# Performance work log

Hardware: AMD Instinct MI355X
Metric: run time of the kernel (lower is better)

## Reference

```python
import jax, jax.numpy as jnp
import numpy as np

N_NODES = 100000
N_EDGES = 1600000
D_FEAT = 128
UNITS = 128


def setup_inputs() -> dict:
    key = jax.random.key(0)
    k = jax.random.split(key, 7)
    x = jax.random.normal(k[0], (N_NODES, D_FEAT), dtype=jnp.float32)
    edge_row = jax.random.randint(k[1], (N_EDGES,), 0, N_NODES, dtype=jnp.int32)
    edge_col = jax.random.randint(k[2], (N_EDGES,), 0, N_NODES, dtype=jnp.int32)
    edge_vals = jax.random.uniform(k[3], (N_EDGES,), dtype=jnp.float32)
    W = jax.random.normal(k[4], (D_FEAT, UNITS), dtype=jnp.float32) * 0.05
    W_gate = jax.random.normal(k[5], (D_FEAT, 1), dtype=jnp.float32) * 0.05
    b_gate = jax.random.normal(k[6], (1,), dtype=jnp.float32) * 0.05
    return {"x": x, "edge_row": edge_row, "edge_col": edge_col,
            "edge_vals": edge_vals, "W": W, "W_gate": W_gate, "b_gate": b_gate}


def reference(x, edge_row, edge_col, edge_vals, W, W_gate, b_gate):
    # pre_sup = X @ W  -> [N, units]
    pre_sup = x @ W
    # gate g = sigmoid(X @ W_gate + b_gate)  -> [N, 1]
    g = jax.nn.sigmoid(x @ W_gate + b_gate)
    h = g * pre_sup  # [N, units]
    # output = A @ h, A in COO form (row, col, vals):
    # out[r] = sum_e vals[e] * h[col[e]] for edges with row[e] == r
    msgs = edge_vals[:, None] * h[edge_col]  # [E, units]
    out = jax.ops.segment_sum(msgs, edge_row, num_segments=N_NODES)
    # activation is None (linear)
    return out
```

## Files before the change

kernel.cpp:

```cpp
#include <hip/hip_runtime.h>
#include <hip/hip_bf16.h>

constexpr int D        = 128;
constexpr int BM       = 64;
constexpr int CHUNK    = 4096;
constexpr int NBKT_PAD = 1024;
constexpr int BKT_CAP  = 3072;
constexpr int BKT_STRIDE = 4096;
constexpr int OVF_CAP  = 65536;
constexpr int EPT      = CHUNK / 256;

typedef __attribute__((ext_vector_type(8))) short bf16x8;
typedef __attribute__((ext_vector_type(4))) float f32x4;

__device__ __forceinline__ unsigned short rne_bf16(float f) {
    unsigned u = __float_as_uint(f);
    return (unsigned short)((u + 0x7FFF + ((u >> 16) & 1)) >> 16);
}

__global__ __launch_bounds__(256) void transpose_W(
    const float* __restrict__ W, unsigned short* __restrict__ wt_sw)
{
    int idx = blockIdx.x * 256 + threadIdx.x;
    int k = idx >> 7, f = idx & 127;
    wt_sw[f * 128 + (k ^ ((f & 7) << 3))] = rne_bf16(W[idx]);
}

__global__ __launch_bounds__(256) void gemm_bin(
    const float* __restrict__ x, const unsigned short* __restrict__ wt_sw,
    const float* __restrict__ Wg, const float* __restrict__ bg,
    __hip_bfloat16* __restrict__ h,
    const int* __restrict__ er, const int* __restrict__ ec,
    const float* __restrict__ ev, int* __restrict__ gcursor,
    uint2* __restrict__ bucketArr, int* __restrict__ ovfCur,
    uint4* __restrict__ ovfArr,
    int n_nodes, int n_edges, int gemm_blocks)
{
    __shared__ __align__(16) char smem[53264];

    const int t    = threadIdx.x;
    const int lane = t & 63;
    const int w    = t >> 6;

    if ((int)blockIdx.x < gemm_blocks) {
        unsigned short* Ahi = (unsigned short*)smem;
        unsigned short* Bt  = Ahi + 64 * 128;
        float*          Gs  = (float*)(Bt + 128 * 128);
        unsigned short* Cbuf = (unsigned short*)smem;

        const int node0 = blockIdx.x * BM;

        #pragma unroll
        for (int i = 0; i < 8; ++i) {
            int e0 = (i * 256 + t) * 8;
            *(int4*)&Bt[e0] = *(const int4*)&wt_sw[e0];
        }

        #pragma unroll
        for (int i = 0; i < 8; ++i) {
            int fidx = (i * 256 + t) * 4;
            int row  = fidx >> 7;
            int k    = fidx & 127;
            int node = node0 + row;
            float4 v = make_float4(0.f, 0.f, 0.f, 0.f);
            if (node < n_nodes) v = *(const float4*)(x + (size_t)node * D + k);
            unsigned long long pk =
                (unsigned long long)rne_bf16(v.x) |
                ((unsigned long long)rne_bf16(v.y) << 16) |
                ((unsigned long long)rne_bf16(v.z) << 32) |
                ((unsigned long long)rne_bf16(v.w) << 48);
            int eidx = row * 128 + (k ^ ((row & 7) << 3));
            *(unsigned long long*)&Ahi[eidx] = pk;
        }
        __syncthreads();

        if (t < BM) {
            float gp = 0.f;
            #pragma unroll
            for (int kq = 0; kq < 16; ++kq) {
                int eidx = t * 128 + ((kq * 8) ^ ((t & 7) << 3));
                unsigned long long a = *(const unsigned long long*)&Ahi[eidx];
                unsigned long long b = *(const unsigned long long*)&Ahi[eidx + 4];
                #pragma unroll
                for (int j = 0; j < 4; ++j) {
                    gp += __uint_as_float((unsigned)((a >> (16 * j)) & 0xFFFF) << 16) * Wg[kq * 8 + j];
                    gp += __uint_as_float((unsigned)((b >> (16 * j)) & 0xFFFF) << 16) * Wg[kq * 8 + 4 + j];
                }
            }
            Gs[t] = 1.f / (1.f + __expf(-(gp + bg[0])));
        }

        f32x4 acc[4][2];
        #pragma unroll
        for (int m = 0; m < 4; ++m)
            #pragma unroll
            for (int n = 0; n < 2; ++n)
                acc[m][n] = (f32x4){0.f, 0.f, 0.f, 0.f};

        #pragma unroll
        for (int kk = 0; kk < 4; ++kk) {
            const int k0 = kk * 32 + (lane >> 4) * 8;
            bf16x8 bfr[2];
            #pragma unroll
            for (int n = 0; n < 2; ++n) {
                int f = w * 32 + n * 16 + (lane & 15);
                bfr[n] = *(const bf16x8*)&Bt[f * 128 + (k0 ^ ((f & 7) << 3))];
            }
            #pragma unroll
            for (int m = 0; m < 4; ++m) {
                int row = m * 16 + (lane & 15);
                bf16x8 ah = *(const bf16x8*)&Ahi[row * 128 + (k0 ^ ((row & 7) << 3))];
                #pragma unroll
                for (int n = 0; n < 2; ++n)
                    acc[m][n] = __builtin_amdgcn_mfma_f32_16x16x32_bf16(ah, bfr[n], acc[m][n], 0, 0, 0);
            }
        }
        __syncthreads();

        #pragma unroll
        for (int m = 0; m < 4; ++m) {
            #pragma unroll
            for (int n = 0; n < 2; ++n) {
                int feat = w * 32 + n * 16 + (lane & 15);
                #pragma unroll
                for (int j = 0; j < 4; ++j) {
                    int rloc = m * 16 + (lane >> 4) * 4 + j;
                    Cbuf[rloc * 136 + feat] = rne_bf16(acc[m][n][j] * Gs[rloc]);
                }
            }
        }
        __syncthreads();

        {
            int row  = t >> 2;
            int fb   = (t & 3) * 32;
            int node = node0 + row;
            if (node < n_nodes) {
                __hip_bfloat16* hp = h + (size_t)node * D + fb;
                #pragma unroll
                for (int q = 0; q < 4; ++q)
                    *(int4*)(hp + q * 8) = *(const int4*)&Cbuf[row * 136 + fb + q * 8];
            }
        }
    } else {
        uint2* staged           = (uint2*)smem;
        unsigned short* bkt_of  = (unsigned short*)(smem + 32768);
        int* lcnt               = (int*)(smem + 40960);
        int* lbase              = lcnt + NBKT_PAD;
        int* gbase              = lbase + NBKT_PAD;
        int* wt                 = gbase + NBKT_PAD;

        const int bb = (int)blockIdx.x - gemm_blocks;
        const int e0 = bb * CHUNK;
        const int ecnt = min(CHUNK, n_edges - e0);

        for (int i = t; i < NBKT_PAD; i += 256) lcnt[i] = 0;
        __syncthreads();

        int rcache[EPT];
        #pragma unroll
        for (int j = 0; j < EPT; ++j) {
            int i = t + j * 256;
            if (i < ecnt) {
                rcache[j] = er[e0 + i];
                atomicAdd(&lcnt[rcache[j] >> 7], 1);
            } else rcache[j] = -1;
        }
        __syncthreads();

        {
            const int base = t * 4;
            int v[4], tsum = 0;
            #pragma unroll
            for (int j = 0; j < 4; ++j) { v[j] = lcnt[base + j]; tsum += v[j]; }
            int x2 = tsum;
            #pragma unroll
            for (int d = 1; d < 64; d <<= 1) {
                int y = __shfl_up(x2, d);
                if (lane >= d) x2 += y;
            }
            if (lane == 63) wt[w] = x2;
            __syncthreads();
            int woff = 0;
            for (int i = 0; i < w; ++i) woff += wt[i];
            int run = woff + x2 - tsum;
            #pragma unroll
            for (int j = 0; j < 4; ++j) { lbase[base + j] = run; run += v[j]; lcnt[base + j] = 0; }
        }
        __syncthreads();

        #pragma unroll
        for (int j = 0; j < EPT; ++j) {
            int i = t + j * 256;
            if (rcache[j] >= 0) {
                int r = rcache[j];
                int b = r >> 7;
                int p = lbase[b] + atomicAdd(&lcnt[b], 1);
                staged[p] = make_uint2((unsigned)ec[e0 + i] | ((unsigned)(r & 127) << 17),
                                       (unsigned)__float_as_int(ev[e0 + i]));
                bkt_of[p] = (unsigned short)b;
            }
        }
        __syncthreads();

        for (int i = t; i < NBKT_PAD; i += 256) {
            int c = lcnt[i];
            if (c) gbase[i] = atomicAdd(&gcursor[i], c);
        }
        __syncthreads();

        for (int i = t; i < ecnt; i += 256) {
            int b = bkt_of[i];
            int pos = gbase[b] + (i - lbase[b]);
            uint2 pe = staged[i];
            if (pos < BKT_STRIDE) {
                bucketArr[(size_t)b * BKT_STRIDE + pos] = pe;
            } else {
                int op = atomicAdd(ovfCur, 1);
                if (op < OVF_CAP) ovfArr[op] = make_uint4((unsigned)b, pe.x, pe.y, 0u);
            }
        }
    }
}

__global__ __launch_bounds__(256) void sort_gather(
    const int* __restrict__ gcursor, const uint2* __restrict__ bucketArr,
    const int* __restrict__ ovfCur, const uint4* __restrict__ ovfArr,
    const __hip_bfloat16* __restrict__ h, float* __restrict__ out, int n_nodes)
{
    __shared__ uint2 sEdges[BKT_CAP];
    __shared__ int rcnt[128];
    __shared__ int rbase[129];
    __shared__ int rfill[128];
    __shared__ int wt2[2];

    const int t = threadIdx.x, lane = t & 63, w = t >> 6;
    const int b = blockIdx.x;
    const int r0 = b << 7;
    const size_t s = (size_t)b * BKT_STRIDE;
    const int total = gcursor[b];
    const int cnt = min(total, BKT_STRIDE);
    const bool ovf = cnt > BKT_CAP;
    const int ovfN = (total > BKT_STRIDE || *ovfCur > 0) ? min(*ovfCur, OVF_CAP) : 0;

    if (t < 128) rcnt[t] = 0;
    __syncthreads();

    if (!ovf) {
        for (int i = t; i < cnt; i += 256)
            atomicAdd(&rcnt[(bucketArr[s + i].x >> 17) & 127], 1);
    }
    __syncthreads();

    {
        int v = 0, x = 0;
        if (t < 128) {
            v = rcnt[t];
            x = v;
            #pragma unroll
            for (int d = 1; d < 64; d <<= 1) {
                int y = __shfl_up(x, d);
                if (lane >= d) x += y;
            }
            if (lane == 63) wt2[w] = x;
        }
        __syncthreads();
        if (t < 128) {
            int rb = (w ? wt2[0] : 0) + x - v;
            rbase[t] = rb;
            rfill[t] = rb;
        }
        if (t == 0) rbase[128] = cnt;
    }
    __syncthreads();

    if (!ovf) {
        for (int i = t; i < cnt; i += 256) {
            uint2 pe = bucketArr[s + i];
            int rl = (pe.x >> 17) & 127;
            int p  = atomicAdd(&rfill[rl], 1);
            sEdges[p] = pe;
        }
    }
    __syncthreads();

    const int g = lane >> 4;
    const int p = lane & 15;

    for (int k = 0; k < 32; ++k) {
        const int rl = w + (k << 2);
        const int row = r0 + rl;
        if (row >= n_nodes) continue;

        float acc[8];
        #pragma unroll
        for (int j = 0; j < 8; ++j) acc[j] = 0.f;

        if (!ovf) {
            const int rs = rbase[rl], re = rbase[rl + 1];
            for (int bb = rs; bb < re; bb += 8) {
                int i0 = bb + g;
                int i1 = i0 + 4;
                float v0 = 0.f, v1 = 0.f;
                int c0 = 0, c1 = 0;
                if (i0 < re) { uint2 pk = sEdges[i0]; v0 = __uint_as_float(pk.y); c0 = (int)(pk.x & 0x1FFFFu); }
                if (i1 < re) { uint2 pk = sEdges[i1]; v1 = __uint_as_float(pk.y); c1 = (int)(pk.x & 0x1FFFFu); }
                const int4 h0 = *(const int4*)(h + (size_t)c0 * D + p * 8);
                const int4 h1 = *(const int4*)(h + (size_t)c1 * D + p * 8);
                {
                    unsigned d0 = (unsigned)h0.x, d1 = (unsigned)h0.y, d2 = (unsigned)h0.z, d3 = (unsigned)h0.w;
                    acc[0] += v0 * __uint_as_float(d0 << 16);
                    acc[1] += v0 * __uint_as_float(d0 & 0xFFFF0000u);
                    acc[2] += v0 * __uint_as_float(d1 << 16);
                    acc[3] += v0 * __uint_as_float(d1 & 0xFFFF0000u);
                    acc[4] += v0 * __uint_as_float(d2 << 16);
                    acc[5] += v0 * __uint_as_float(d2 & 0xFFFF0000u);
                    acc[6] += v0 * __uint_as_float(d3 << 16);
                    acc[7] += v0 * __uint_as_float(d3 & 0xFFFF0000u);
                }
                {
                    unsigned d0 = (unsigned)h1.x, d1 = (unsigned)h1.y, d2 = (unsigned)h1.z, d3 = (unsigned)h1.w;
                    acc[0] += v1 * __uint_as_float(d0 << 16);
                    acc[1] += v1 * __uint_as_float(d0 & 0xFFFF0000u);
                    acc[2] += v1 * __uint_as_float(d1 << 16);
                    acc[3] += v1 * __uint_as_float(d1 & 0xFFFF0000u);
                    acc[4] += v1 * __uint_as_float(d2 << 16);
                    acc[5] += v1 * __uint_as_float(d2 & 0xFFFF0000u);
                    acc[6] += v1 * __uint_as_float(d3 << 16);
                    acc[7] += v1 * __uint_as_float(d3 & 0xFFFF0000u);
                }
            }
        } else {
            const unsigned target = (unsigned)rl;
            for (int bb = 0; bb < cnt; bb += 8) {
                int i0 = bb + g;
                int i1 = i0 + 4;
                float v0 = 0.f, v1 = 0.f;
                int c0 = 0, c1 = 0;
                if (i0 < cnt) {
                    uint2 pk = bucketArr[s + i0];
                    if (((pk.x >> 17) & 127u) == target) { v0 = __uint_as_float(pk.y); c0 = (int)(pk.x & 0x1FFFFu); }
                }
                if (i1 < cnt) {
                    uint2 pk = bucketArr[s + i1];
                    if (((pk.x >> 17) & 127u) == target) { v1 = __uint_as_float(pk.y); c1 = (int)(pk.x & 0x1FFFFu); }
                }
                const int4 h0 = *(const int4*)(h + (size_t)c0 * D + p * 8);
                const int4 h1 = *(const int4*)(h + (size_t)c1 * D + p * 8);
                {
                    unsigned d0 = (unsigned)h0.x, d1 = (unsigned)h0.y, d2 = (unsigned)h0.z, d3 = (unsigned)h0.w;
                    acc[0] += v0 * __uint_as_float(d0 << 16);
                    acc[1] += v0 * __uint_as_float(d0 & 0xFFFF0000u);
                    acc[2] += v0 * __uint_as_float(d1 << 16);
                    acc[3] += v0 * __uint_as_float(d1 & 0xFFFF0000u);
                    acc[4] += v0 * __uint_as_float(d2 << 16);
                    acc[5] += v0 * __uint_as_float(d2 & 0xFFFF0000u);
                    acc[6] += v0 * __uint_as_float(d3 << 16);
                    acc[7] += v0 * __uint_as_float(d3 & 0xFFFF0000u);
                }
                {
                    unsigned d0 = (unsigned)h1.x, d1 = (unsigned)h1.y, d2 = (unsigned)h1.z, d3 = (unsigned)h1.w;
                    acc[0] += v1 * __uint_as_float(d0 << 16);
                    acc[1] += v1 * __uint_as_float(d0 & 0xFFFF0000u);
                    acc[2] += v1 * __uint_as_float(d1 << 16);
                    acc[3] += v1 * __uint_as_float(d1 & 0xFFFF0000u);
                    acc[4] += v1 * __uint_as_float(d2 << 16);
                    acc[5] += v1 * __uint_as_float(d2 & 0xFFFF0000u);
                    acc[6] += v1 * __uint_as_float(d3 << 16);
                    acc[7] += v1 * __uint_as_float(d3 & 0xFFFF0000u);
                }
            }
        }

        if (ovfN > 0 && g == 0) {
            for (int j = 0; j < ovfN; ++j) {
                uint4 oe = ovfArr[j];
                if (oe.x == (unsigned)b && ((oe.y >> 17) & 127u) == (unsigned)rl) {
                    float v = __uint_as_float(oe.z);
                    int col = (int)(oe.y & 0x1FFFFu);
                    const int4 hv = *(const int4*)(h + (size_t)col * D + p * 8);
                    unsigned d0 = (unsigned)hv.x, d1 = (unsigned)hv.y, d2 = (unsigned)hv.z, d3 = (unsigned)hv.w;
                    acc[0] += v * __uint_as_float(d0 << 16);
                    acc[1] += v * __uint_as_float(d0 & 0xFFFF0000u);
                    acc[2] += v * __uint_as_float(d1 << 16);
                    acc[3] += v * __uint_as_float(d1 & 0xFFFF0000u);
                    acc[4] += v * __uint_as_float(d2 << 16);
                    acc[5] += v * __uint_as_float(d2 & 0xFFFF0000u);
                    acc[6] += v * __uint_as_float(d3 << 16);
                    acc[7] += v * __uint_as_float(d3 & 0xFFFF0000u);
                }
            }
        }

        #pragma unroll
        for (int j = 0; j < 8; ++j) {
            acc[j] += __shfl_xor(acc[j], 16);
            acc[j] += __shfl_xor(acc[j], 32);
        }

        if (lane < 16) {
            float* op = out + (size_t)row * D + lane * 8;
            *(float4*)(op)     = make_float4(acc[0], acc[1], acc[2], acc[3]);
            *(float4*)(op + 4) = make_float4(acc[4], acc[5], acc[6], acc[7]);
        }
    }
}

__global__ __launch_bounds__(256) void scatter_edges(
    const int* __restrict__ er, const int* __restrict__ ec,
    const float* __restrict__ ev, const __hip_bfloat16* __restrict__ h,
    float* __restrict__ out, int n_edges)
{
    int gw   = (blockIdx.x * 256 + threadIdx.x) >> 6;
    int lane = threadIdx.x & 63;
    if (gw >= n_edges) return;
    int r = er[gw];
    int c = ec[gw];
    float v = ev[gw];
    unsigned hv = *(const unsigned*)(h + (size_t)c * D + lane * 2);
    float* op = out + (size_t)r * D + lane * 2;
    atomicAdd(op,     v * __uint_as_float(hv << 16));
    atomicAdd(op + 1, v * __uint_as_float(hv & 0xFFFF0000u));
}

__global__ __launch_bounds__(256) void mfma_gemm_only(
    const float* __restrict__ x, const unsigned short* __restrict__ wt_sw,
    const float* __restrict__ Wg, const float* __restrict__ bg,
    __hip_bfloat16* __restrict__ h, int n_nodes)
{
}

extern "C" void kernel_launch(void* const* d_in, const int* in_sizes, int n_in,
                              void* d_out, int out_size, void* d_ws, size_t ws_size,
                              hipStream_t stream) {
    const float* x  = (const float*)d_in[0];
    const int*   er = (const int*)d_in[1];
    const int*   ec = (const int*)d_in[2];
    const float* ev = (const float*)d_in[3];
    const float* W  = (const float*)d_in[4];
    const float* Wg = (const float*)d_in[5];
    const float* bg = (const float*)d_in[6];
    float* out = (float*)d_out;

    const int n_nodes = in_sizes[0] / D;
    const int n_edges = in_sizes[1];
    const int nbkt = (n_nodes + 127) >> 7;
    const int gemm_blocks = (n_nodes + BM - 1) / BM;
    const int bin_blocks  = (n_edges + CHUNK - 1) / CHUNK;

    char* ws = (char*)d_ws;
    size_t off = 0;
    auto alloc = [&](size_t bytes) {
        char* p = ws + off;
        off += (bytes + 15) & ~size_t(15);
        return p;
    };
    __hip_bfloat16* h = (__hip_bfloat16*)alloc((size_t)n_nodes * D * sizeof(__hip_bfloat16));
    unsigned short* wt_sw = (unsigned short*)alloc((size_t)D * D * sizeof(unsigned short));
    uint2* bucketArr = (uint2*)alloc((size_t)nbkt * BKT_STRIDE * sizeof(uint2));
    int*   gcursor   = (int*)  alloc(NBKT_PAD * sizeof(int));
    int*   ovfCur    = (int*)  alloc(16);
    uint4* ovfArr    = (uint4*)alloc((size_t)OVF_CAP * sizeof(uint4));
    bool have_ws = off <= ws_size;

    transpose_W<<<D * D / 256, 256, 0, stream>>>(W, wt_sw);

    if (have_ws) {
        hipMemsetAsync(gcursor, 0, NBKT_PAD * sizeof(int) + 16, stream);
        gemm_bin<<<gemm_blocks + bin_blocks, 256, 0, stream>>>(
            x, wt_sw, Wg, bg, h, er, ec, ev, gcursor, bucketArr, ovfCur, ovfArr,
            n_nodes, n_edges, gemm_blocks);
        sort_gather<<<nbkt, 256, 0, stream>>>(gcursor, bucketArr, ovfCur, ovfArr, h, out, n_nodes);
    } else {
        gemm_bin<<<gemm_blocks, 256, 0, stream>>>(
            x, wt_sw, Wg, bg, h, er, ec, ev, (int*)nullptr, (uint2*)nullptr,
            (int*)nullptr, (uint4*)nullptr, n_nodes, n_edges, gemm_blocks);
        hipMemsetAsync(d_out, 0, (size_t)out_size * sizeof(float), stream);
        int blocks = (n_edges + 3) / 4;
        scatter_edges<<<blocks, 256, 0, stream>>>(er, ec, ev, h, out, n_edges);
    }
}
```

Measured before the change: 126.3 us.

## Shrink fused gemm/bin LDS footprint, read W from global, direct-scatter edges

The GEMM half no longer stages the transposed W in shared memory; each wave reads B fragments directly from global/L2, cutting LDS from about 52KB to about 17KB so more blocks can be resident. The binning half reserves global bucket slots during the prefix scan and writes each edge straight to its bucket, removing the LDS staging buffer and two barrier phases. It also launches the bin blocks first and caches bucket entries in registers in sort_gather to avoid reading them twice. The trade-off is uncoalesced, unswizzled global reads of W in the MFMA loop and more scattered global writes when binning edges.

```diff
diff --git a/kernel.cpp b/kernel.cpp
--- a/kernel.cpp
+++ b/kernel.cpp
@@ -19,42 +19,35 @@
 }
 
 __global__ __launch_bounds__(256) void transpose_W(
-    const float* __restrict__ W, unsigned short* __restrict__ wt_sw)
+    const float* __restrict__ W, unsigned short* __restrict__ wt)
 {
     int idx = blockIdx.x * 256 + threadIdx.x;
     int k = idx >> 7, f = idx & 127;
-    wt_sw[f * 128 + (k ^ ((f & 7) << 3))] = rne_bf16(W[idx]);
+    wt[f * 128 + k] = rne_bf16(W[idx]);
 }
 
 __global__ __launch_bounds__(256) void gemm_bin(
-    const float* __restrict__ x, const unsigned short* __restrict__ wt_sw,
+    const float* __restrict__ x, const unsigned short* __restrict__ wt,
     const float* __restrict__ Wg, const float* __restrict__ bg,
     __hip_bfloat16* __restrict__ h,
     const int* __restrict__ er, const int* __restrict__ ec,
     const float* __restrict__ ev, int* __restrict__ gcursor,
     uint2* __restrict__ bucketArr, int* __restrict__ ovfCur,
     uint4* __restrict__ ovfArr,
-    int n_nodes, int n_edges, int gemm_blocks)
+    int n_nodes, int n_edges, int bin_blocks)
 {
-    __shared__ __align__(16) char smem[53264];
+    __shared__ __align__(16) char smem[17664];
 
     const int t    = threadIdx.x;
     const int lane = t & 63;
     const int w    = t >> 6;
 
-    if ((int)blockIdx.x < gemm_blocks) {
-        unsigned short* Ahi = (unsigned short*)smem;
-        unsigned short* Bt  = Ahi + 64 * 128;
-        float*          Gs  = (float*)(Bt + 128 * 128);
+    if ((int)blockIdx.x >= bin_blocks) {
+        unsigned short* Ahi  = (unsigned short*)smem;
+        float*          Gs   = (float*)(smem + 17408);
         unsigned short* Cbuf = (unsigned short*)smem;
 
-        const int node0 = blockIdx.x * BM;
-
-        #pragma unroll
-        for (int i = 0; i < 8; ++i) {
-            int e0 = (i * 256 + t) * 8;
-            *(int4*)&Bt[e0] = *(const int4*)&wt_sw[e0];
-        }
+        const int node0 = ((int)blockIdx.x - bin_blocks) * BM;
 
         #pragma unroll
         for (int i = 0; i < 8; ++i) {
@@ -104,7 +97,7 @@
             #pragma unroll
             for (int n = 0; n < 2; ++n) {
                 int f = w * 32 + n * 16 + (lane & 15);
-                bfr[n] = *(const bf16x8*)&Bt[f * 128 + (k0 ^ ((f & 7) << 3))];
+                bfr[n] = *(const bf16x8*)&wt[f * 128 + k0];
             }
             #pragma unroll
             for (int m = 0; m < 4; ++m) {
@@ -143,15 +136,12 @@
             }
         }
     } else {
-        uint2* staged           = (uint2*)smem;
-        unsigned short* bkt_of  = (unsigned short*)(smem + 32768);
-        int* lcnt               = (int*)(smem + 40960);
-        int* lbase              = lcnt + NBKT_PAD;
-        int* gbase              = lbase + NBKT_PAD;
-        int* wt                 = gbase + NBKT_PAD;
-
-        const int bb = (int)blockIdx.x - gemm_blocks;
-        const int e0 = bb * CHUNK;
+        int* lcnt  = (int*)smem;
+        int* lbase = lcnt + NBKT_PAD;
+        int* gbase = lbase + NBKT_PAD;
+        int* wt4   = gbase + NBKT_PAD;
+
+        const int e0 = (int)blockIdx.x * CHUNK;
         const int ecnt = min(CHUNK, n_edges - e0);
 
         for (int i = t; i < NBKT_PAD; i += 256) lcnt[i] = 0;
@@ -179,13 +169,17 @@
                 int y = __shfl_up(x2, d);
                 if (lane >= d) x2 += y;
             }
-            if (lane == 63) wt[w] = x2;
+            if (lane == 63) wt4[w] = x2;
             __syncthreads();
             int woff = 0;
-            for (int i = 0; i < w; ++i) woff += wt[i];
+            for (int i = 0; i < w; ++i) woff += wt4[i];
             int run = woff + x2 - tsum;
             #pragma unroll
-            for (int j = 0; j < 4; ++j) { lbase[base + j] = run; run += v[j]; lcnt[base + j] = 0; }
+            for (int j = 0; j < 4; ++j) {
+                lbase[base + j] = run; run += v[j];
+                if (v[j]) gbase[base + j] = atomicAdd(&gcursor[base + j], v[j]);
+                lcnt[base + j] = 0;
+            }
         }
         __syncthreads();
 
@@ -195,29 +189,16 @@
             if (rcache[j] >= 0) {
                 int r = rcache[j];
                 int b = r >> 7;
-                int p = lbase[b] + atomicAdd(&lcnt[b], 1);
-                staged[p] = make_uint2((unsigned)ec[e0 + i] | ((unsigned)(r & 127) << 17),
-                                       (unsigned)__float_as_int(ev[e0 + i]));
-                bkt_of[p] = (unsigned short)b;
-            }
-        }
-        __syncthreads();
-
-        for (int i = t; i < NBKT_PAD; i += 256) {
-            int c = lcnt[i];
-            if (c) gbase[i] = atomicAdd(&gcursor[i], c);
-        }
-        __syncthreads();
-
-        for (int i = t; i < ecnt; i += 256) {
-            int b = bkt_of[i];
-            int pos = gbase[b] + (i - lbase[b]);
-            uint2 pe = staged[i];
-            if (pos < BKT_STRIDE) {
-                bucketArr[(size_t)b * BKT_STRIDE + pos] = pe;
-            } else {
-                int op = atomicAdd(ovfCur, 1);
-                if (op < OVF_CAP) ovfArr[op] = make_uint4((unsigned)b, pe.x, pe.y, 0u);
+                int rank = atomicAdd(&lcnt[b], 1);
+                int pos  = gbase[b] + rank;
+                uint2 pe = make_uint2((unsigned)ec[e0 + i] | ((unsigned)(r & 127) << 17),
+                                      (unsigned)__float_as_int(ev[e0 + i]));
+                if (pos < BKT_STRIDE) {
+                    bucketArr[(size_t)b * BKT_STRIDE + pos] = pe;
+                } else {
+                    int op = atomicAdd(ovfCur, 1);
+                    if (op < OVF_CAP) ovfArr[op] = make_uint4((unsigned)b, pe.x, pe.y, 0u);
+                }
             }
         }
     }
@@ -246,9 +227,17 @@
     if (t < 128) rcnt[t] = 0;
     __syncthreads();
 
+    uint2 ecache[12];
     if (!ovf) {
-        for (int i = t; i < cnt; i += 256)
-            atomicAdd(&rcnt[(bucketArr[s + i].x >> 17) & 127], 1);
+        #pragma unroll
+        for (int j = 0; j < 12; ++j) {
+            int i = t + j * 256;
+            ecache[j] = (i < cnt) ? bucketArr[s + i] : make_uint2(0xFFFFFFFFu, 0u);
+        }
+        #pragma unroll
+        for (int j = 0; j < 12; ++j)
+            if (ecache[j].x != 0xFFFFFFFFu)
+                atomicAdd(&rcnt[(ecache[j].x >> 17) & 127], 1);
     }
     __syncthreads();
 
@@ -275,11 +264,13 @@
     __syncthreads();
 
     if (!ovf) {
-        for (int i = t; i < cnt; i += 256) {
-            uint2 pe = bucketArr[s + i];
-            int rl = (pe.x >> 17) & 127;
-            int p  = atomicAdd(&rfill[rl], 1);
-            sEdges[p] = pe;
+        #pragma unroll
+        for (int j = 0; j < 12; ++j) {
+            if (ecache[j].x != 0xFFFFFFFFu) {
+                int rl = (ecache[j].x >> 17) & 127;
+                int p  = atomicAdd(&rfill[rl], 1);
+                sEdges[p] = ecache[j];
+            }
         }
     }
     __syncthreads();
@@ -423,13 +414,6 @@
     atomicAdd(op + 1, v * __uint_as_float(hv & 0xFFFF0000u));
 }
 
-__global__ __launch_bounds__(256) void mfma_gemm_only(
-    const float* __restrict__ x, const unsigned short* __restrict__ wt_sw,
-    const float* __restrict__ Wg, const float* __restrict__ bg,
-    __hip_bfloat16* __restrict__ h, int n_nodes)
-{
-}
-
 extern "C" void kernel_launch(void* const* d_in, const int* in_sizes, int n_in,
                               void* d_out, int out_size, void* d_ws, size_t ws_size,
                               hipStream_t stream) {
@@ -456,25 +440,25 @@
         return p;
     };
     __hip_bfloat16* h = (__hip_bfloat16*)alloc((size_t)n_nodes * D * sizeof(__hip_bfloat16));
-    unsigned short* wt_sw = (unsigned short*)alloc((size_t)D * D * sizeof(unsigned short));
+    unsigned short* wt = (unsigned short*)alloc((size_t)D * D * sizeof(unsigned short));
     uint2* bucketArr = (uint2*)alloc((size_t)nbkt * BKT_STRIDE * sizeof(uint2));
     int*   gcursor   = (int*)  alloc(NBKT_PAD * sizeof(int));
     int*   ovfCur    = (int*)  alloc(16);
     uint4* ovfArr    = (uint4*)alloc((size_t)OVF_CAP * sizeof(uint4));
     bool have_ws = off <= ws_size;
 
-    transpose_W<<<D * D / 256, 256, 0, stream>>>(W, wt_sw);
+    transpose_W<<<D * D / 256, 256, 0, stream>>>(W, wt);
 
     if (have_ws) {
         hipMemsetAsync(gcursor, 0, NBKT_PAD * sizeof(int) + 16, stream);
-        gemm_bin<<<gemm_blocks + bin_blocks, 256, 0, stream>>>(
-            x, wt_sw, Wg, bg, h, er, ec, ev, gcursor, bucketArr, ovfCur, ovfArr,
-            n_nodes, n_edges, gemm_blocks);
+        gemm_bin<<<bin_blocks + gemm_blocks, 256, 0, stream>>>(
+            x, wt, Wg, bg, h, er, ec, ev, gcursor, bucketArr, ovfCur, ovfArr,
+            n_nodes, n_edges, bin_blocks);
         sort_gather<<<nbkt, 256, 0, stream>>>(gcursor, bucketArr, ovfCur, ovfArr, h, out, n_nodes);
     } else {
         gemm_bin<<<gemm_blocks, 256, 0, stream>>>(
-            x, wt_sw, Wg, bg, h, er, ec, ev, (int*)nullptr, (uint2*)nullptr,
-            (int*)nullptr, (uint4*)nullptr, n_nodes, n_edges, gemm_blocks);
+            x, wt, Wg, bg, h, er, ec, ev, (int*)nullptr, (uint2*)nullptr,
+            (int*)nullptr, (uint4*)nullptr, n_nodes, n_edges, 0);
         hipMemsetAsync(d_out, 0, (size_t)out_size * sizeof(float), stream);
         int blocks = (n_edges + 3) / 4;
         scatter_edges<<<blocks, 256, 0, stream>>>(er, ec, ev, h, out, n_edges);
```

Result: slower. 139.1 us (+10.2%).
